# Kernel tuning notes

Measured on AMD Instinct MI355X. Metric: run time of the kernel, lower is better.

## Reference

```python
import jax, jax.numpy as jnp
import numpy as np

ALPHA = 0.1  # history blend factor from __init__


def _grid_sample_border(tex_t, grid):
    """Bilinear grid_sample, align_corners=False, padding_mode='border'.
    tex_t: [N,H,W,C] (channels-last), grid: [N,Hg,Wg,2] with (x,y) in [-1,1].
    Returns [N,Hg,Wg,C].
    """
    N, H, W, C = tex_t.shape
    x = (grid[..., 0] + 1.0) * (W * 0.5) - 0.5  # pixel coords
    y = (grid[..., 1] + 1.0) * (H * 0.5) - 0.5
    x0f = jnp.floor(x)
    y0f = jnp.floor(y)
    wx = (x - x0f)[..., None]
    wy = (y - y0f)[..., None]
    x0 = jnp.clip(x0f.astype(jnp.int32), 0, W - 1)
    x1 = jnp.clip(x0f.astype(jnp.int32) + 1, 0, W - 1)
    y0 = jnp.clip(y0f.astype(jnp.int32), 0, H - 1)
    y1 = jnp.clip(y0f.astype(jnp.int32) + 1, 0, H - 1)
    b = jnp.arange(N)[:, None, None]
    v00 = tex_t[b, y0, x0]
    v01 = tex_t[b, y0, x1]
    v10 = tex_t[b, y1, x0]
    v11 = tex_t[b, y1, x1]
    top = v00 * (1.0 - wx) + v01 * wx
    bot = v10 * (1.0 - wx) + v11 * wx
    return top * (1.0 - wy) + bot * wy


def _bicubic_grid_sample(tex, grid):
    """Catmull-Rom 5-tap bicubic sampling (matches torch BiCubicGridSample).
    tex: [N,C,H,W], grid: [N,Hg,Wg,2]. Returns [N,C,Hg,Wg].
    The torch code appends an all-ones alpha channel before weighting; since
    bilinear sampling of a constant-1 channel is 1, the alpha accumulator
    equals the sum of the 5 scalar weights, which we compute directly.
    """
    N, C, H, W = tex.shape
    tex_t = jnp.transpose(tex, (0, 2, 3, 1))  # NHWC
    ws = jnp.array([W, H], dtype=tex.dtype)
    rws = 1.0 / ws
    uv = (grid + 1.0) * 0.5
    pos = uv * ws
    cpos = jnp.floor(pos - 0.5) + 0.5
    f = pos - cpos
    f2 = f * f
    f3 = f2 * f
    w0 = -0.5 * f3 + f2 - 0.5 * f
    w2 = -1.5 * f3 + 2.0 * f2 + 0.5 * f
    w3 = 0.5 * f3 - 0.5 * f2
    w12 = (1.5 * f3 - 2.5 * f2 + 1.0) + w2  # w1 + w2
    tc12 = rws * (cpos + w2 / w12)
    tc0 = rws * (cpos - 1.0)
    tc3 = rws * (cpos + 2.0)

    def samp(uvx, uvy):
        g = (jnp.stack([uvx, uvy], axis=-1) - 0.5) * 2.0
        return _grid_sample_border(tex_t, g)  # [N,Hg,Wg,C]

    # scalar per-pixel weights
    ww1 = w12[..., 0] * w0[..., 1]
    ww2 = w0[..., 0] * w12[..., 1]
    ww3 = w3[..., 0] * w12[..., 1]
    ww4 = w12[..., 0] * w3[..., 1]
    ww5 = w12[..., 0] * w12[..., 1]

    out = (samp(tc12[..., 0], tc0[..., 1]) * ww1[..., None]
           + samp(tc0[..., 0], tc12[..., 1]) * ww2[..., None]
           + samp(tc3[..., 0], tc12[..., 1]) * ww3[..., None]
           + samp(tc12[..., 0], tc3[..., 1]) * ww4[..., None]
           + samp(tc12[..., 0], tc12[..., 1]) * ww5[..., None])
    rec = (ww1 + ww2 + ww3 + ww4 + ww5)[..., None]
    out = out / rec
    return jnp.transpose(out, (0, 3, 1, 2))  # NCHW


def _max_pool3(x):
    # 3x3 max pool, stride 1, padding 1 on NCHW
    return jax.lax.reduce_window(x, -jnp.inf, jax.lax.max,
                                 (1, 1, 3, 3), (1, 1, 1, 1), 'SAME')


def setup_inputs() -> dict:
    key = jax.random.key(0)
    k1, k2, k3 = jax.random.split(key, 3)
    N, C, H, W = 2, 3, 1080, 1920
    x = jax.random.uniform(k1, (N, C, H, W), dtype=jnp.float32)
    history = jax.random.uniform(k2, (N, C, H, W), dtype=jnp.float32)
    # motion-vector grid: roughly identity UVs with small per-pixel jitter
    gy, gx = jnp.meshgrid(
        (jnp.arange(H, dtype=jnp.float32) + 0.5) / H * 2.0 - 1.0,
        (jnp.arange(W, dtype=jnp.float32) + 0.5) / W * 2.0 - 1.0,
        indexing='ij')
    base = jnp.stack([gx, gy], axis=-1)[None]  # [1,H,W,2]
    jitter = (jax.random.uniform(k3, (N, H, W, 2), dtype=jnp.float32) - 0.5) * 0.01
    mv = base + jitter
    return {"x": x, "mv": mv, "history": history}


def reference(x, mv, history):
    reproj = _bicubic_grid_sample(history, mv)
    max_nh = _max_pool3(x)
    min_nh = -_max_pool3(-x)
    reproj = jnp.minimum(jnp.maximum(reproj, min_nh), max_nh)
    return ALPHA * x + (1.0 - ALPHA) * reproj
```

## Files before the change

kernel.cpp:

```cpp
#include <hip/hip_runtime.h>

static constexpr float ALPHA = 0.1f;

typedef _Float16 h2 __attribute__((ext_vector_type(2)));

#define TW 64
#define TH 8
#define HROWS 16
#define HCOLS 84
#define NTEX (HROWS * HCOLS)

__device__ __forceinline__ int iclamp(int v, int lo, int hi) { return min(max(v, lo), hi); }

__device__ __forceinline__ unsigned pk(float a, float b) {
    return __builtin_bit_cast(unsigned, __builtin_amdgcn_cvt_pkrtz(a, b));
}
__device__ __forceinline__ h2 toh2(unsigned u) { return __builtin_bit_cast(h2, u); }
__device__ __forceinline__ h2 bc2(float v) { return toh2(pk(v, v)); }

struct Setup {
    int mA, m1, m2, mB;
    float t, w0, w3, w12;
};

__device__ __forceinline__ Setup axis_setup(float gcoord, float S) {
    Setup s;
    float pos = (gcoord + 1.0f) * 0.5f * S;
    float pm  = floorf(pos - 0.5f);
    float f   = pos - (pm + 0.5f);
    float f2 = f * f, f3 = f2 * f;
    s.w0  = -0.5f * f3 + f2 - 0.5f * f;
    float w2 = -1.5f * f3 + 2.0f * f2 + 0.5f * f;
    s.w3  =  0.5f * f3 - 0.5f * f2;
    s.w12 = (1.5f * f3 - 2.5f * f2 + 1.0f) + w2;
    float p12 = pm + __fdividef(w2, s.w12);
    float fl  = floorf(p12);
    s.t = p12 - fl;
    int m = (int)pm, i12 = (int)fl;
    s.mA = m - 1; s.m1 = i12; s.m2 = i12 + 1; s.mB = m + 2;
    return s;
}

__global__ __launch_bounds__(256, 4) void taa_kernel(
    const float* __restrict__ x, const float* __restrict__ mv,
    const float* __restrict__ hist, float* __restrict__ out)
{
    constexpr int N = 2, H = 1080, W = 1920, HW = H * W;
    constexpr int NTX = W / TW;
    constexpr int NTY = H / TH;
    constexpr int NWG = N * NTX * NTY;
    constexpr int Q = NWG / 8, R = NWG % 8;

    __shared__ __align__(8) uint2 Lh[NTEX];

    int d = blockIdx.x;
    int xcd = d & 7, di = d >> 3;
    int work = (xcd < R ? xcd * (Q + 1) : R * (Q + 1) + (xcd - R) * Q) + di;
    int n   = work / (NTX * NTY);
    int rem = work - n * (NTX * NTY);
    int ty  = rem / NTX;
    int tx  = rem - ty * NTX;
    const int w0 = tx * TW, h0 = ty * TH;

    const int lx = threadIdx.x & 63;
    const int wv = threadIdx.x >> 6;
    const int wpix = w0 + lx;
    const int hbase = h0 + 2 * wv;

    const float* hn = hist + n * 3 * HW;
    const float* xn = x    + n * 3 * HW;

    const float2 g0 = ((const float2*)mv)[n * HW + hbase * W + wpix];
    const float2 g1 = ((const float2*)mv)[n * HW + (hbase + 1) * W + wpix];

    const bool interior = (tx >= 1) && (tx <= NTX - 2) &&
                          (h0 >= 4) && (h0 + TH + 3 <= H - 1);
    if (interior) {
        for (int idx = threadIdx.x; idx < NTEX; idx += 256) {
            int r  = idx / HCOLS;
            int cc = idx - r * HCOLS;
            const float* src = hn + (h0 - 4 + r) * W + (w0 - 8) + cc;
            Lh[idx] = make_uint2(pk(src[0], src[HW]), pk(src[2 * HW], 0.0f));
        }
    } else {
        for (int idx = threadIdx.x; idx < NTEX; idx += 256) {
            int r  = idx / HCOLS;
            int cc = idx - r * HCOLS;
            int gr = iclamp(h0 - 4 + r, 0, H - 1);
            int gc = iclamp(w0 - 8 + cc, 0, W - 1);
            const float* src = hn + gr * W + gc;
            Lh[idx] = make_uint2(pk(src[0], src[HW]), pk(src[2 * HW], 0.0f));
        }
    }

    int rg0 = iclamp(hbase - 1, 0, H - 1) * W;
    int rg1 = hbase * W;
    int rg2 = (hbase + 1) * W;
    int rg3 = iclamp(hbase + 2, 0, H - 1) * W;
    const int rg[4] = {rg0, rg1, rg2, rg3};

    float hmx[3][4], hmn[3][4], xmid[3][4];
    if (tx >= 1 && tx <= NTX - 2) {
#pragma unroll
        for (int c = 0; c < 3; ++c) {
            const float* xc = xn + c * HW + wpix;
#pragma unroll
            for (int rr = 0; rr < 4; ++rr) {
                const float* p = xc + rg[rr];
                float a = p[-1], b = p[0], e = p[1];
                hmx[c][rr]  = fmaxf(fmaxf(a, b), e);
                hmn[c][rr]  = fminf(fminf(a, b), e);
                xmid[c][rr] = b;
            }
        }
    } else {
        const int wm = max(wpix - 1, 0), wp = min(wpix + 1, W - 1);
#pragma unroll
        for (int c = 0; c < 3; ++c) {
            const float* xc = xn + c * HW;
#pragma unroll
            for (int rr = 0; rr < 4; ++rr) {
                float a = xc[rg[rr] + wm];
                float b = xc[rg[rr] + wpix];
                float e = xc[rg[rr] + wp];
                hmx[c][rr]  = fmaxf(fmaxf(a, b), e);
                hmn[c][rr]  = fminf(fminf(a, b), e);
                xmid[c][rr] = b;
            }
        }
    }

    Setup sx0 = axis_setup(g0.x, (float)W);
    Setup sy0 = axis_setup(g0.y, (float)H);
    Setup sx1 = axis_setup(g1.x, (float)W);
    Setup sy1 = axis_setup(g1.y, (float)H);

    __syncthreads();

    float* on = out + n * 3 * HW;

#pragma unroll
    for (int p = 0; p < 2; ++p) {
        const Setup& sx = p ? sx1 : sx0;
        const Setup& sy = p ? sy1 : sy0;

        const int lrA = iclamp(sy.mA - (h0 - 4), 0, HROWS - 1);
        const int lr1 = iclamp(sy.m1 - (h0 - 4), 0, HROWS - 1);
        const int lr2 = iclamp(sy.m2 - (h0 - 4), 0, HROWS - 1);
        const int lrB = iclamp(sy.mB - (h0 - 4), 0, HROWS - 1);
        const int lcA = iclamp(sx.mA - (w0 - 8), 0, HCOLS - 1);
        const int lc1 = iclamp(sx.m1 - (w0 - 8), 0, HCOLS - 1);
        const int lc2 = iclamp(sx.m2 - (w0 - 8), 0, HCOLS - 1);
        const int lcB = iclamp(sx.mB - (w0 - 8), 0, HCOLS - 1);

        const int rA = lrA * HCOLS, r1 = lr1 * HCOLS, r2 = lr2 * HCOLS, rB = lrB * HCOLS;

        uint2 tA1 = Lh[rA + lc1], tA2 = Lh[rA + lc2];
        uint2 tB1 = Lh[rB + lc1], tB2 = Lh[rB + lc2];
        uint2 tL1 = Lh[r1 + lcA], tL2 = Lh[r2 + lcA];
        uint2 tR1 = Lh[r1 + lcB], tR2 = Lh[r2 + lcB];
        uint2 tC11 = Lh[r1 + lc1], tC12 = Lh[r1 + lc2];
        uint2 tC21 = Lh[r2 + lc1], tC22 = Lh[r2 + lc2];

        const float tx_ = sx.t, ty_ = sy.t;
        const float omtx = 1.0f - tx_, omty = 1.0f - ty_;
        const float ww1 = sx.w12 * sy.w0;
        const float ww2 = sx.w0  * sy.w12;
        const float ww3 = sx.w3  * sy.w12;
        const float ww4 = sx.w12 * sy.w3;
        const float ww5 = sx.w12 * sy.w12;
        const float rrec = __fdividef(1.0f, ww1 + ww2 + ww3 + ww4 + ww5);

        const h2 htx = bc2(tx_),  homtx = bc2(omtx);
        const h2 hty = bc2(ty_),  homty = bc2(omty);
        const h2 hw1 = bc2(ww1), hw2 = bc2(ww2), hw3 = bc2(ww3),
                 hw4 = bc2(ww4), hw5 = bc2(ww5);

#define H2PAIR(T) toh2(T.x), toh2(T.y)
        h2 A1rg = toh2(tA1.x), A1bp = toh2(tA1.y), A2rg = toh2(tA2.x), A2bp = toh2(tA2.y);
        h2 B1rg = toh2(tB1.x), B1bp = toh2(tB1.y), B2rg = toh2(tB2.x), B2bp = toh2(tB2.y);
        h2 L1rg = toh2(tL1.x), L1bp = toh2(tL1.y), L2rg = toh2(tL2.x), L2bp = toh2(tL2.y);
        h2 R1rg = toh2(tR1.x), R1bp = toh2(tR1.y), R2rg = toh2(tR2.x), R2bp = toh2(tR2.y);
        h2 C11rg = toh2(tC11.x), C11bp = toh2(tC11.y), C12rg = toh2(tC12.x), C12bp = toh2(tC12.y);
        h2 C21rg = toh2(tC21.x), C21bp = toh2(tC21.y), C22rg = toh2(tC22.x), C22bp = toh2(tC22.y);

        h2 s1rg = A1rg * homtx + A2rg * htx,  s1bp = A1bp * homtx + A2bp * htx;
        h2 s4rg = B1rg * homtx + B2rg * htx,  s4bp = B1bp * homtx + B2bp * htx;
        h2 s2rg = L1rg * homty + L2rg * hty,  s2bp = L1bp * homty + L2bp * hty;
        h2 s3rg = R1rg * homty + R2rg * hty,  s3bp = R1bp * homty + R2bp * hty;
        h2 s5rg = (C11rg * homtx + C12rg * htx) * homty + (C21rg * homtx + C22rg * htx) * hty;
        h2 s5bp = (C11bp * homtx + C12bp * htx) * homty + (C21bp * homtx + C22bp * htx) * hty;

        h2 accrg = s1rg * hw1 + s2rg * hw2 + s3rg * hw3 + s4rg * hw4 + s5rg * hw5;
        h2 accbp = s1bp * hw1 + s2bp * hw2 + s3bp * hw3 + s4bp * hw4 + s5bp * hw5;

        float rv[3] = { (float)accrg[0] * rrec, (float)accrg[1] * rrec, (float)accbp[0] * rrec };

        const int gpix = (hbase + p) * W + wpix;
#pragma unroll
        for (int c = 0; c < 3; ++c) {
            float mxv = fmaxf(fmaxf(hmx[c][p], hmx[c][p + 1]), hmx[c][p + 2]);
            float mnv = fminf(fminf(hmn[c][p], hmn[c][p + 1]), hmn[c][p + 2]);
            float reproj = fminf(fmaxf(rv[c], mnv), mxv);
            on[c * HW + gpix] = ALPHA * xmid[c][p + 1] + (1.0f - ALPHA) * reproj;
        }
    }
}

extern "C" void kernel_launch(void* const* d_in, const int* in_sizes, int n_in,
                              void* d_out, int out_size, void* d_ws, size_t ws_size,
                              hipStream_t stream) {
    const float* x    = (const float*)d_in[0];
    const float* mv   = (const float*)d_in[1];
    const float* hist = (const float*)d_in[2];
    float* out = (float*)d_out;

    constexpr int NWG = 2 * (1920 / TW) * (1080 / TH);
    taa_kernel<<<dim3(NWG, 1, 1), dim3(256, 1, 1), 0, stream>>>(x, mv, hist, out);
}
```

Measured before the change: 43.82 us.

## Enlarge tile to 12 rows with three output rows per thread

Raises the tile height from 8 to 12 rows, so each wavefront handles three output rows instead of two and the shared history halo grows from 16 to 20 rows. This lowers the relative halo overhead for both the shared-memory history tile and the 3x3 neighbourhood loads of x, and halves the XCD remainder handling since the workgroup count now divides by 8. The cost is more registers per thread, a larger LDS footprint, and fewer workgroups, which may reduce occupancy and load balance.

```diff
diff --git a/kernel.cpp b/kernel.cpp
--- a/kernel.cpp
+++ b/kernel.cpp
@@ -5,8 +5,8 @@
 typedef _Float16 h2 __attribute__((ext_vector_type(2)));
 
 #define TW 64
-#define TH 8
-#define HROWS 16
+#define TH 12
+#define HROWS 20
 #define HCOLS 84
 #define NTEX (HROWS * HCOLS)
 
@@ -19,7 +19,7 @@
 __device__ __forceinline__ h2 bc2(float v) { return toh2(pk(v, v)); }
 
 struct Setup {
-    int mA, m1, m2, mB;
+    int mA, m1, mB;
     float t, w0, w3, w12;
 };
 
@@ -36,8 +36,9 @@
     float p12 = pm + __fdividef(w2, s.w12);
     float fl  = floorf(p12);
     s.t = p12 - fl;
-    int m = (int)pm, i12 = (int)fl;
-    s.mA = m - 1; s.m1 = i12; s.m2 = i12 + 1; s.mB = m + 2;
+    s.m1 = (int)fl;
+    int m = (int)pm;
+    s.mA = m - 1; s.mB = m + 2;
     return s;
 }
 
@@ -49,13 +50,12 @@
     constexpr int NTX = W / TW;
     constexpr int NTY = H / TH;
     constexpr int NWG = N * NTX * NTY;
-    constexpr int Q = NWG / 8, R = NWG % 8;
+    constexpr int Q = NWG / 8;
 
     __shared__ __align__(8) uint2 Lh[NTEX];
 
     int d = blockIdx.x;
-    int xcd = d & 7, di = d >> 3;
-    int work = (xcd < R ? xcd * (Q + 1) : R * (Q + 1) + (xcd - R) * Q) + di;
+    int work = (d & 7) * Q + (d >> 3);
     int n   = work / (NTX * NTY);
     int rem = work - n * (NTX * NTY);
     int ty  = rem / NTX;
@@ -65,13 +65,14 @@
     const int lx = threadIdx.x & 63;
     const int wv = threadIdx.x >> 6;
     const int wpix = w0 + lx;
-    const int hbase = h0 + 2 * wv;
+    const int hbase = h0 + 3 * wv;
 
     const float* hn = hist + n * 3 * HW;
     const float* xn = x    + n * 3 * HW;
 
     const float2 g0 = ((const float2*)mv)[n * HW + hbase * W + wpix];
     const float2 g1 = ((const float2*)mv)[n * HW + (hbase + 1) * W + wpix];
+    const float2 g2 = ((const float2*)mv)[n * HW + (hbase + 2) * W + wpix];
 
     const bool interior = (tx >= 1) && (tx <= NTX - 2) &&
                           (h0 >= 4) && (h0 + TH + 3 <= H - 1);
@@ -96,21 +97,22 @@
     int rg0 = iclamp(hbase - 1, 0, H - 1) * W;
     int rg1 = hbase * W;
     int rg2 = (hbase + 1) * W;
-    int rg3 = iclamp(hbase + 2, 0, H - 1) * W;
-    const int rg[4] = {rg0, rg1, rg2, rg3};
-
-    float hmx[3][4], hmn[3][4], xmid[3][4];
+    int rg3 = (hbase + 2) * W;
+    int rg4 = iclamp(hbase + 3, 0, H - 1) * W;
+    const int rg[5] = {rg0, rg1, rg2, rg3, rg4};
+
+    float hmx[3][5], hmn[3][5], xmid[3][3];
     if (tx >= 1 && tx <= NTX - 2) {
 #pragma unroll
         for (int c = 0; c < 3; ++c) {
             const float* xc = xn + c * HW + wpix;
 #pragma unroll
-            for (int rr = 0; rr < 4; ++rr) {
+            for (int rr = 0; rr < 5; ++rr) {
                 const float* p = xc + rg[rr];
                 float a = p[-1], b = p[0], e = p[1];
                 hmx[c][rr]  = fmaxf(fmaxf(a, b), e);
                 hmn[c][rr]  = fminf(fminf(a, b), e);
-                xmid[c][rr] = b;
+                if (rr >= 1 && rr <= 3) xmid[c][rr - 1] = b;
             }
         }
     } else {
@@ -119,13 +121,13 @@
         for (int c = 0; c < 3; ++c) {
             const float* xc = xn + c * HW;
 #pragma unroll
-            for (int rr = 0; rr < 4; ++rr) {
+            for (int rr = 0; rr < 5; ++rr) {
                 float a = xc[rg[rr] + wm];
                 float b = xc[rg[rr] + wpix];
                 float e = xc[rg[rr] + wp];
                 hmx[c][rr]  = fmaxf(fmaxf(a, b), e);
                 hmn[c][rr]  = fminf(fminf(a, b), e);
-                xmid[c][rr] = b;
+                if (rr >= 1 && rr <= 3) xmid[c][rr - 1] = b;
             }
         }
     }
@@ -134,24 +136,26 @@
     Setup sy0 = axis_setup(g0.y, (float)H);
     Setup sx1 = axis_setup(g1.x, (float)W);
     Setup sy1 = axis_setup(g1.y, (float)H);
+    Setup sx2 = axis_setup(g2.x, (float)W);
+    Setup sy2 = axis_setup(g2.y, (float)H);
 
     __syncthreads();
 
     float* on = out + n * 3 * HW;
 
 #pragma unroll
-    for (int p = 0; p < 2; ++p) {
-        const Setup& sx = p ? sx1 : sx0;
-        const Setup& sy = p ? sy1 : sy0;
-
-        const int lrA = iclamp(sy.mA - (h0 - 4), 0, HROWS - 1);
-        const int lr1 = iclamp(sy.m1 - (h0 - 4), 0, HROWS - 1);
-        const int lr2 = iclamp(sy.m2 - (h0 - 4), 0, HROWS - 1);
-        const int lrB = iclamp(sy.mB - (h0 - 4), 0, HROWS - 1);
-        const int lcA = iclamp(sx.mA - (w0 - 8), 0, HCOLS - 1);
-        const int lc1 = iclamp(sx.m1 - (w0 - 8), 0, HCOLS - 1);
-        const int lc2 = iclamp(sx.m2 - (w0 - 8), 0, HCOLS - 1);
-        const int lcB = iclamp(sx.mB - (w0 - 8), 0, HCOLS - 1);
+    for (int p = 0; p < 3; ++p) {
+        const Setup& sx = (p == 0) ? sx0 : (p == 1) ? sx1 : sx2;
+        const Setup& sy = (p == 0) ? sy0 : (p == 1) ? sy1 : sy2;
+
+        const int lrA = iclamp(sy.mA     - (h0 - 4), 0, HROWS - 1);
+        const int lr1 = iclamp(sy.m1     - (h0 - 4), 0, HROWS - 1);
+        const int lr2 = iclamp(sy.m1 + 1 - (h0 - 4), 0, HROWS - 1);
+        const int lrB = iclamp(sy.mB     - (h0 - 4), 0, HROWS - 1);
+        const int lcA = iclamp(sx.mA     - (w0 - 8), 0, HCOLS - 1);
+        const int lc1 = iclamp(sx.m1     - (w0 - 8), 0, HCOLS - 1);
+        const int lc2 = iclamp(sx.m1 + 1 - (w0 - 8), 0, HCOLS - 1);
+        const int lcB = iclamp(sx.mB     - (w0 - 8), 0, HCOLS - 1);
 
         const int rA = lrA * HCOLS, r1 = lr1 * HCOLS, r2 = lr2 * HCOLS, rB = lrB * HCOLS;
 
@@ -176,7 +180,6 @@
         const h2 hw1 = bc2(ww1), hw2 = bc2(ww2), hw3 = bc2(ww3),
                  hw4 = bc2(ww4), hw5 = bc2(ww5);
 
-#define H2PAIR(T) toh2(T.x), toh2(T.y)
         h2 A1rg = toh2(tA1.x), A1bp = toh2(tA1.y), A2rg = toh2(tA2.x), A2bp = toh2(tA2.y);
         h2 B1rg = toh2(tB1.x), B1bp = toh2(tB1.y), B2rg = toh2(tB2.x), B2bp = toh2(tB2.y);
         h2 L1rg = toh2(tL1.x), L1bp = toh2(tL1.y), L2rg = toh2(tL2.x), L2bp = toh2(tL2.y);
@@ -202,7 +205,7 @@
             float mxv = fmaxf(fmaxf(hmx[c][p], hmx[c][p + 1]), hmx[c][p + 2]);
             float mnv = fminf(fminf(hmn[c][p], hmn[c][p + 1]), hmn[c][p + 2]);
             float reproj = fminf(fmaxf(rv[c], mnv), mxv);
-            on[c * HW + gpix] = ALPHA * xmid[c][p + 1] + (1.0f - ALPHA) * reproj;
+            on[c * HW + gpix] = ALPHA * xmid[c][p] + (1.0f - ALPHA) * reproj;
         }
     }
 }
```

Result: slower. 46.98 us (+7.2%).
